# Performance work log

Measured on AMD Instinct MI355X. Metric: run time of the kernel, lower is better.

## Reference

```python
import jax, jax.numpy as jnp
import numpy as np

V, E, H = 30000, 512, 512
MARGIN = 0.05


def _lstm(x, wih, whh, b):
    # x: [N,T,E]; torch LSTM gate order i,f,g,o; returns outputs [N,T,H]
    N = x.shape[0]
    Hh = whh.shape[1]
    xproj = jnp.swapaxes(x, 0, 1) @ wih.T + b  # [T,N,4H], input proj hoisted out of scan

    def step(carry, xp):
        h, c = carry
        g = xp + h @ whh.T
        i, f, gg, o = jnp.split(g, 4, axis=-1)
        c = jax.nn.sigmoid(f) * c + jax.nn.sigmoid(i) * jnp.tanh(gg)
        h = jax.nn.sigmoid(o) * jnp.tanh(c)
        return (h, c), h

    h0 = jnp.zeros((N, Hh), x.dtype)
    _, hs = jax.lax.scan(step, (h0, h0), xproj)
    return jnp.swapaxes(hs, 0, 1)


def _attn_pool(feat, lengths, aw, ab, sw, sb):
    # batched masked-softmax attention pooling (replaces per-sample python loop)
    T = feat.shape[1]
    s = (jnp.tanh(feat @ aw.T + ab) @ sw.T + sb)[..., 0]  # [N,T]
    mask = jnp.arange(T)[None, :] < lengths[:, None]
    w = jax.nn.softmax(jnp.where(mask, s, -1e30), axis=1)
    return jnp.einsum('nt,nth->nh', w, feat)  # [N,H]


def _cos(a, b, eps=1e-8):
    na = jnp.maximum(jnp.linalg.norm(a, axis=-1), eps)
    nb = jnp.maximum(jnp.linalg.norm(b, axis=-1), eps)
    return jnp.sum(a * b, axis=-1) / (na * nb)


def setup_inputs() -> dict:
    key = jax.random.key(0)
    ks = jax.random.split(key, 24)
    B, BL, T, TD = 32, 8, 128, 256
    d = {}
    d['tran'] = jax.random.randint(ks[0], (B, BL, T), 1, V)
    d['tran_len'] = jax.random.randint(ks[1], (B,), 1, T + 1)
    d['tran_block_len'] = jax.random.randint(ks[2], (B, BL), 1, T + 1)
    d['doc_anchor'] = jax.random.randint(ks[3], (B, TD), 1, V)
    d['doc_anchor_len'] = jax.random.randint(ks[4], (B,), 1, TD + 1)
    d['doc_neg'] = jax.random.randint(ks[5], (B, TD), 1, V)
    d['doc_neg_len'] = jax.random.randint(ks[6], (B,), 1, TD + 1)
    sc = 0.05
    emb = jax.random.normal(ks[7], (V, E), jnp.float32) * sc
    d['emb'] = emb.at[0].set(0.0)  # padding_idx=0
    d['tran_wih'] = jax.random.normal(ks[8], (4 * H, E), jnp.float32) * sc
    d['tran_whh'] = jax.random.normal(ks[9], (4 * H, H), jnp.float32) * sc
    d['tran_b'] = jax.random.normal(ks[10], (4 * H,), jnp.float32) * sc
    d['doc_wih'] = jax.random.normal(ks[11], (4 * H, E), jnp.float32) * sc
    d['doc_whh'] = jax.random.normal(ks[12], (4 * H, H), jnp.float32) * sc
    d['doc_b'] = jax.random.normal(ks[13], (4 * H,), jnp.float32) * sc
    d['tran_attn_w'] = jax.random.normal(ks[14], (H, H), jnp.float32) * sc
    d['tran_attn_b'] = jax.random.normal(ks[15], (H,), jnp.float32) * sc
    d['tran_s_w'] = jax.random.normal(ks[16], (1, H), jnp.float32) * sc
    d['tran_s_b'] = jax.random.normal(ks[17], (1,), jnp.float32) * sc
    d['doc_attn_w'] = jax.random.normal(ks[18], (H, H), jnp.float32) * sc
    d['doc_attn_b'] = jax.random.normal(ks[19], (H,), jnp.float32) * sc
    d['doc_s_w'] = jax.random.normal(ks[20], (1, H), jnp.float32) * sc
    d['doc_s_b'] = jax.random.normal(ks[21], (1,), jnp.float32) * sc
    return d


def reference(tran, tran_len, tran_block_len, doc_anchor, doc_anchor_len,
              doc_neg, doc_neg_len, emb, tran_wih, tran_whh, tran_b,
              doc_wih, doc_whh, doc_b, tran_attn_w, tran_attn_b,
              tran_s_w, tran_s_b, doc_attn_w, doc_attn_b, doc_s_w, doc_s_b):
    B, BL, T = tran.shape
    # --- code side: encode B*BL sub-sequences, attn pool, tanh, max over block ---
    flat = tran.reshape(B * BL, T)
    feat = _lstm(emb[flat], tran_wih, tran_whh, tran_b)  # [B*BL,T,H]
    pooled = _attn_pool(feat, tran_block_len.reshape(-1),
                        tran_attn_w, tran_attn_b, tran_s_w, tran_s_b)
    pooled = jnp.tanh(pooled)  # use_tanh on attn output (tran path)
    code_repr = jnp.max(pooled.reshape(B, BL, H), axis=1)  # max_pool over block

    # --- doc side: attn pool, no trailing tanh (doc_encoding has no use_tanh branch) ---
    def doc_enc(tok, lens):
        f = _lstm(emb[tok], doc_wih, doc_whh, doc_b)
        return _attn_pool(f, lens, doc_attn_w, doc_attn_b, doc_s_w, doc_s_b)

    da = doc_enc(doc_anchor, doc_anchor_len)
    dn = doc_enc(doc_neg, doc_neg_len)

    anchor_sim = _cos(code_repr, da)
    neg_sim = _cos(code_repr, dn)
    loss = jnp.mean(jnp.clip(MARGIN - anchor_sim + neg_sim, 1e-6, None))
    return loss
```

## Files before the change

kernel.cpp:

```cpp
#include <hip/hip_runtime.h>
#include <hip/hip_bf16.h>

#define NSEQ 320
#define NTRAN 256
#define TT 128
#define TDOC 256
#define EH 512
#define XR_TRAN (NTRAN*TT)
#define XROWS (XR_TRAN + 64*TDOC)
#define HSLOTS 6
#define FW 264

typedef __attribute__((ext_vector_type(8))) short bf16x8v;
typedef __attribute__((ext_vector_type(4))) float f32x4v;

__device__ __align__(16) unsigned short g_xb [(size_t)XROWS*EH];
__device__ __align__(16) unsigned short g_wbx[2*2048*512];
__device__ __align__(16) unsigned short g_w2b[2*5*512*512];
__device__ float g_xp[(size_t)XROWS*2048];
__device__ float g_h [HSLOTS*NSEQ*EH];
__device__ float g_sc[64*260];
__device__ float g_pool[NSEQ*EH];
__device__ float g_loss;
__device__ unsigned g_gflag[48*FW];
__device__ unsigned g_sflag[16*FW];
__device__ unsigned g_aprog[48];

__device__ __forceinline__ float sigm(float x) { return 1.0f / (1.0f + expf(-x)); }

__device__ __forceinline__ float ldg_sys(const float* p) {
  return __hip_atomic_load(p, __ATOMIC_RELAXED, __HIP_MEMORY_SCOPE_SYSTEM);
}
__device__ __forceinline__ void stg_sys(float* p, float v) {
  __hip_atomic_store(p, v, __ATOMIC_RELAXED, __HIP_MEMORY_SCOPE_SYSTEM);
}
__device__ __forceinline__ unsigned ldu(const unsigned* p) {
  return __hip_atomic_load(p, __ATOMIC_RELAXED, __HIP_MEMORY_SCOPE_AGENT);
}
__device__ __forceinline__ unsigned short f2b(float f) {
  __hip_bfloat16 h = __float2bfloat16(f);
  return *reinterpret_cast<unsigned short*>(&h);
}

__global__ __launch_bounds__(256) void init_state() {
  int i = blockIdx.x*256 + threadIdx.x;
  if (i < NSEQ*EH) g_h[5*NSEQ*EH + i] = 0.0f;
  if (i < 64*260) g_sc[i] = 0.0f;
  if (i < 48*FW) g_gflag[i] = ((i % FW) == 0) ? 4u : 0u;
  if (i < 16*FW) g_sflag[i] = 0u;
  if (i < 48) g_aprog[i] = 0u;
  if (i == 0) g_loss = 0.0f;
}

__global__ __launch_bounds__(256) void build_wbx(
    const float* __restrict__ wih_t, const float* __restrict__ wih_d) {
  int idx = blockIdx.x*256 + threadIdx.x;
  if (idx >= 2*2048*512) return;
  int p = idx / (2048*512); int rem = idx % (2048*512);
  const float* wih = p ? wih_d : wih_t;
  g_wbx[idx] = f2b(wih[rem]);
}

__global__ __launch_bounds__(256) void build_wt2(
    const float* __restrict__ whh_t, const float* __restrict__ whh_d,
    const float* __restrict__ aw_t,  const float* __restrict__ aw_d) {
  int idx = blockIdx.x*256 + threadIdx.x;
  if (idx >= 2*5*512*512) return;
  int p  = idx / (5*512*512); int rem = idx % (5*512*512);
  int cg = rem / (512*512);   int r2  = rem % (512*512);
  int k  = r2 >> 9;           int c   = r2 & 511;
  float v;
  if (cg < 4) {
    int r = (c >> 7)*512 + cg*128 + (c & 127);
    const float* whh = p ? whh_d : whh_t;
    v = whh[r*512 + k];
  } else {
    const float* aw = p ? aw_d : aw_t;
    v = aw[c*512 + k];
  }
  g_w2b[((size_t)(p*5 + cg)*512 + k)*512 + c] = f2b(v);
}

__global__ __launch_bounds__(128) void pregather(
    const int* __restrict__ tran, const int* __restrict__ da_tok,
    const int* __restrict__ dn_tok, const float* __restrict__ emb) {
  int row = blockIdx.x;
  int tok;
  if (row < XR_TRAN) tok = tran[row];
  else {
    int q = row - XR_TRAN;
    tok = (q < 32*TDOC) ? da_tok[q] : dn_tok[q - 32*TDOC];
  }
  const float4* src = (const float4*)&emb[(size_t)tok*EH];
  float4 v = src[threadIdx.x];
  uint2 o;
  o.x = (unsigned)f2b(v.x) | ((unsigned)f2b(v.y) << 16);
  o.y = (unsigned)f2b(v.z) | ((unsigned)f2b(v.w) << 16);
  ((uint2*)&g_xb[(size_t)row*EH])[threadIdx.x] = o;
}

__global__ __launch_bounds__(512, 2) void xproj_mfma(
    const float* __restrict__ b_t, const float* __restrict__ b_d) {
  __shared__ short As[2][256*32];
  __shared__ short Bs[2][256*32];
  const int bid = blockIdx.x;
  const int mt = bid >> 3, ntb = bid & 7;
  const size_t mb = (size_t)mt * 256; const int nb = ntb * 256;
  const bool tp = (mb < XR_TRAN);
  const size_t wboff = (tp ? 0 : (size_t)2048*512);
  const float* __restrict__ bias = tp ? b_t : b_d;
  const int tid = threadIdx.x;
  const int l = tid & 63, w = tid >> 6;
  const int mw = w >> 2, nw = w & 3;

  f32x4v acc[8][4];
  #pragma unroll
  for (int m2 = 0; m2 < 8; ++m2)
    #pragma unroll
    for (int n2 = 0; n2 < 4; ++n2) acc[m2][n2] = (f32x4v){0.f, 0.f, 0.f, 0.f};

  uint4 rA[2], rB[2];
  auto stage_load = [&](int k0) {
    #pragma unroll
    for (int i = 0; i < 2; ++i) {
      int u = i*512 + tid;
      rA[i] = *(const uint4*)&g_xb[(mb + (u >> 2))*512 + k0 + (u & 3)*8];
      rB[i] = *(const uint4*)&g_wbx[wboff + (size_t)(nb + (u >> 2))*512 + k0 + (u & 3)*8];
    }
  };
  auto stage_write = [&](int buf) {
    #pragma unroll
    for (int i = 0; i < 2; ++i) {
      int u = i*512 + tid;
      *(uint4*)&As[buf][u*8] = rA[i];
      *(uint4*)&Bs[buf][u*8] = rB[i];
    }
  };

  stage_load(0); stage_write(0); __syncthreads();
  for (int ks = 0; ks < 16; ++ks) {
    const int buf = ks & 1;
    if (ks < 15) stage_load((ks + 1)*32);
    bf16x8v aF[8], bF[4];
    #pragma unroll
    for (int m2 = 0; m2 < 8; ++m2)
      aF[m2] = *(const bf16x8v*)&As[buf][(mw*128 + m2*16 + (l & 15))*32 + (l >> 4)*8];
    #pragma unroll
    for (int n2 = 0; n2 < 4; ++n2)
      bF[n2] = *(const bf16x8v*)&Bs[buf][(nw*64 + n2*16 + (l & 15))*32 + (l >> 4)*8];
    #pragma unroll
    for (int m2 = 0; m2 < 8; ++m2)
      #pragma unroll
      for (int n2 = 0; n2 < 4; ++n2)
        acc[m2][n2] = __builtin_amdgcn_mfma_f32_16x16x32_bf16(aF[m2], bF[n2], acc[m2][n2], 0, 0, 0);
    __syncthreads();
    if (ks < 15) stage_write(buf ^ 1);
    __syncthreads();
  }

  #pragma unroll
  for (int n2 = 0; n2 < 4; ++n2) {
    const int colg = nb + nw*64 + n2*16 + (l & 15);
    const int col2 = ((colg & 511) >> 7)*512 + (colg >> 9)*128 + (colg & 127);
    const float bv = bias[colg];
    #pragma unroll
    for (int m2 = 0; m2 < 8; ++m2) {
      #pragma unroll
      for (int r = 0; r < 4; ++r) {
        size_t row = mb + mw*128 + m2*16 + (l >> 4)*4 + r;
        g_xp[row*2048 + col2] = acc[m2][n2][r] + bv;
      }
    }
  }
}

template<int S, int CPL>
__device__ __forceinline__ void gemm2(const unsigned short* __restrict__ wsl,
                                      const float* __restrict__ ht,
                                      float* __restrict__ part,
                                      int kq, int lane) {
  constexpr int PW = CPL*64 + 4;
  float acc[CPL][S];
  #pragma unroll
  for (int c = 0; c < CPL; ++c)
    #pragma unroll
    for (int s = 0; s < S; ++s) acc[c][s] = 0.0f;
  const unsigned short* wp = wsl + (size_t)(kq*64)*512 + CPL*lane;
  const float* hb = ht + kq*64;
  #pragma unroll 2
  for (int k4 = 0; k4 < 16; ++k4) {
    float4 hv[S];
    #pragma unroll
    for (int s = 0; s < S; ++s) hv[s] = *(const float4*)&hb[s*516 + k4*4];
    #pragma unroll
    for (int i4 = 0; i4 < 4; ++i4) {
      float wf[CPL];
      if constexpr (CPL == 8) {
        uint4 wv = *(const uint4*)(wp + (size_t)(k4*4 + i4)*512);
        wf[0] = __uint_as_float(wv.x << 16); wf[1] = __uint_as_float(wv.x & 0xFFFF0000u);
        wf[2] = __uint_as_float(wv.y << 16); wf[3] = __uint_as_float(wv.y & 0xFFFF0000u);
        wf[4] = __uint_as_float(wv.z << 16); wf[5] = __uint_as_float(wv.z & 0xFFFF0000u);
        wf[6] = __uint_as_float(wv.w << 16); wf[7] = __uint_as_float(wv.w & 0xFFFF0000u);
      } else {
        uint2 wv = *(const uint2*)(wp + (size_t)(k4*4 + i4)*512);
        wf[0] = __uint_as_float(wv.x << 16); wf[1] = __uint_as_float(wv.x & 0xFFFF0000u);
        wf[2] = __uint_as_float(wv.y << 16); wf[3] = __uint_as_float(wv.y & 0xFFFF0000u);
      }
      #pragma unroll
      for (int s = 0; s < S; ++s) {
        float h = ((const float*)&hv[s])[i4];
        #pragma unroll
        for (int c = 0; c < CPL; ++c) acc[c][s] = fmaf(wf[c], h, acc[c][s]);
      }
    }
  }
  if (kq < 4) {
    #pragma unroll
    for (int s = 0; s < S; ++s)
      #pragma unroll
      for (int c = 0; c < CPL; ++c)
        part[(size_t)(kq*S + s)*PW + CPL*lane + c] = acc[c][s];
  }
  __syncthreads();
  if (kq >= 4) {
    const int q = kq - 4;
    #pragma unroll
    for (int s = 0; s < S; ++s)
      #pragma unroll
      for (int c = 0; c < CPL; ++c)
        part[(size_t)(q*S + s)*PW + CPL*lane + c] += acc[c][s];
  }
}

__global__ __launch_bounds__(512, 2) void persist(
    const int* __restrict__ tbl, const int* __restrict__ dal, const int* __restrict__ dnl,
    const float* __restrict__ ab_t, const float* __restrict__ ab_d,
    const float* __restrict__ sw_t, const float* __restrict__ sw_d,
    const float* __restrict__ sb_t, const float* __restrict__ sb_d) {
  __shared__ float sm[28920];
  float* part = sm;
  float* ht   = sm + 16512;
  float* cb   = sm + 20640;
  float* scr  = sm + 24736;
  float* ml   = sm + 24752;
  float* lenb = sm + 24768;
  float* alb  = sm + 24776;
  float* htB  = sm + 24792;

  const int b = blockIdx.x, tid = threadIdx.x;
  const int x = b & 7, m = b >> 3;
  bool tran; int cg, nt;
  if (x < 5) { tran = true; cg = x; nt = m; }
  else { int slot = (x - 5)*32 + m; tran = false; cg = slot >> 4; nt = slot & 15; }
  const int S     = tran ? 8 : 4;
  const int Ts    = tran ? TT : TDOC;
  const int sbase = tran ? nt*8 : NTRAN + nt*4;
  const bool isattn = (cg >= 4);
  const int gr = tran ? nt : 32 + nt;
  const unsigned AK = tran ? 1u : 2u;
  const int colbase = tran ? 0 : (cg - 4) * 256;
  const int wslice  = isattn ? 4 : cg;
  const unsigned short* __restrict__ wsl =
      g_w2b + (size_t)((tran ? 0 : 5) + wslice)*512*512 + (isattn ? colbase : 0);
  const float* __restrict__ ab  = tran ? ab_t : ab_d;
  const float* __restrict__ sw  = tran ? sw_t : sw_d;
  const float  sb = tran ? sb_t[0] : sb_d[0];

  for (int i = tid; i < 4096; i += 512) cb[i] = 0.0f;
  if (tid < S) {
    ml[tid*2] = -3.0e38f; ml[tid*2+1] = 0.0f;
    int s = sbase + tid;
    int len = tran ? tbl[s] : (s < NTRAN+32 ? dal[s-NTRAN] : dnl[s-NTRAN-32]);
    lenb[tid] = (float)len;
  }
  __syncthreads();

  const int lane = tid & 63, kq = tid >> 6;
  const int w = kq;
  const int PW = tran ? 516 : (isattn ? 260 : 516);
  const int CW = isattn ? (tran ? 512 : 256) : 0;
  const int DW = isattn ? (tran ? 512 : 256) : 0;

  if (!isattn) {
    for (int t = 0; t < Ts; ++t) {
      float xpA[4], xpB[4];
      {
        int i = tid; int jl = i & 127, s = i >> 7;
        size_t row = tran ? (size_t)(sbase + s)*TT + t
                          : (size_t)XR_TRAN + (size_t)(sbase + s - NTRAN)*TDOC + t;
        const float* xr = &g_xp[row*2048 + cg*512];
        #pragma unroll
        for (int g4 = 0; g4 < 4; ++g4) xpA[g4] = xr[g4*128 + jl];
      }
      if (tran) {
        int i = tid + 512; int jl = i & 127, s = i >> 7;
        size_t row = (size_t)(sbase + s)*TT + t;
        const float* xr = &g_xp[row*2048 + cg*512];
        #pragma unroll
        for (int g4 = 0; g4 < 4; ++g4) xpB[g4] = xr[g4*128 + jl];
      }
      if (t > 0)
        while (ldu(&g_gflag[gr*FW + t]) < 4u) __builtin_amdgcn_s_sleep(1);
      if (t >= 5) {
        unsigned tgt = AK * (unsigned)(t - 4);
        while (ldu(&g_aprog[gr]) < tgt) __builtin_amdgcn_s_sleep(1);
      }
      const int sp = (t + 5) % HSLOTS;
      for (int s = 0; s < S; ++s)
        ht[s*516 + kq*64 + lane] =
            ldg_sys(&g_h[((size_t)sp*NSEQ + sbase + s)*EH + kq*64 + lane]);
      if (tran) gemm2<8,8>(wsl, ht, part, kq, lane);
      else      gemm2<4,8>(wsl, ht, part, kq, lane);
      __syncthreads();
      const int so = t % HSLOTS;
      {
        int i = tid; int jl = i & 127, s = i >> 7;
        float u[4];
        #pragma unroll
        for (int g4 = 0; g4 < 4; ++g4) {
          float v = xpA[g4];
          #pragma unroll
          for (int q = 0; q < 4; ++q) v += part[(size_t)(q*S + s)*516 + g4*128 + jl];
          u[g4] = v;
        }
        float cv = cb[s*128 + jl];
        float cn = sigm(u[1])*cv + sigm(u[0])*tanhf(u[2]);
        float hn = sigm(u[3])*tanhf(cn);
        cb[s*128 + jl] = cn;
        stg_sys(&g_h[((size_t)so*NSEQ + sbase + s)*EH + cg*128 + jl], hn);
      }
      if (tran) {
        int i = tid + 512; int jl = i & 127, s = i >> 7;
        float u[4];
        #pragma unroll
        for (int g4 = 0; g4 < 4; ++g4) {
          float v = xpB[g4];
          #pragma unroll
          for (int q = 0; q < 4; ++q) v += part[(size_t)(q*S + s)*516 + g4*128 + jl];
          u[g4] = v;
        }
        float cv = cb[s*128 + jl];
        float cn = sigm(u[1])*cv + sigm(u[0])*tanhf(u[2]);
        float hn = sigm(u[3])*tanhf(cn);
        cb[s*128 + jl] = cn;
        stg_sys(&g_h[((size_t)so*NSEQ + sbase + s)*EH + cg*128 + jl], hn);
      }
      __syncthreads();
      if (tid == 0) atomicAdd(&g_gflag[gr*FW + t + 1], 1u);
    }
  } else {
    for (int t = 1; t <= Ts + 1; ++t) {
      float* hcur  = (t & 1) ? htB : ht;
      float* hprev = (t & 1) ? ht : htB;
      if (tid == 0) {
        if (t <= Ts)
          while (ldu(&g_gflag[gr*FW + t]) < 4u) __builtin_amdgcn_s_sleep(1);
        if (!tran && t >= 2)
          while (ldu(&g_sflag[nt*FW + (t - 1)]) < 2u) __builtin_amdgcn_s_sleep(1);
      }
      __syncthreads();
      const int sp = (t + 5) % HSLOTS;
      if (t <= Ts) {
        for (int s = 0; s < S; ++s)
          hcur[s*516 + kq*64 + lane] =
              ldg_sys(&g_h[((size_t)sp*NSEQ + sbase + s)*EH + kq*64 + lane]);
      }
      if (t >= 2 && tid < S) {
        int s = tid;
        if ((float)(t - 2) < lenb[s]) {
          float sv = tran ? scr[(t & 1)*8 + s]
                          : ldg_sys(&g_sc[(sbase + s - NTRAN)*260 + (t - 2)]);
          float mo = ml[s*2], lo = ml[s*2+1];
          float mn = fmaxf(mo, sv);
          float a = expf(mo - mn), e = expf(sv - mn);
          alb[s*2] = a; alb[s*2+1] = e;
          ml[s*2] = mn; ml[s*2+1] = lo*a + e;
        } else { alb[s*2] = 1.0f; alb[s*2+1] = 0.0f; }
      }
      __syncthreads();
      if (t <= Ts) {
        if (tran) gemm2<8,8>(wsl, hcur, part, kq, lane);
        else      gemm2<4,4>(wsl, hcur, part, kq, lane);
      }
      if (t >= 2) {
        for (int i = tid; i < S*DW; i += 512) {
          int s = tran ? (i >> 9) : (i >> 8);
          int dl = i & (DW - 1);
          float a = alb[s*2], e = alb[s*2+1];
          if (!(a == 1.0f && e == 0.0f)) {
            float hv = hprev[s*516 + colbase + dl];
            cb[s*DW + dl] = cb[s*DW + dl]*a + e*hv;
          }
        }
      }
      __syncthreads();
      if (tid == 0) atomicAdd(&g_aprog[gr], 1u);
      if (t <= Ts) {
        for (int i = tid; i < CW*S; i += 512) {
          int c = i & (CW - 1);
          int s = tran ? (i >> 9) : (i >> 8);
          float u = ab[colbase + c];
          #pragma unroll
          for (int q = 0; q < 4; ++q) u += part[(size_t)(q*S + s)*PW + c];
          float p = tanhf(u) * sw[colbase + c];
          part[(size_t)s*PW + c] = p;
        }
        __syncthreads();
        if (w < S) {
          int s = w;
          float p = 0.0f;
          for (int j = 0; j < CW/64; ++j) p += part[(size_t)s*PW + j*64 + lane];
          #pragma unroll
          for (int off = 32; off >= 1; off >>= 1) p += __shfl_xor(p, off, 64);
          if (lane == 0) {
            if (tran) scr[((t - 1) & 1)*8 + s] = p + sb;
            else atomicAdd(&g_sc[(sbase + s - NTRAN)*260 + (t - 1)],
                           p + (cg == 4 ? sb : 0.0f));
          }
        }
        if (!tran) {
          __syncthreads();
          if (tid == 0) atomicAdd(&g_sflag[nt*FW + t], 1u);
        }
      }
    }
    for (int i = tid; i < S*DW; i += 512) {
      int s = tran ? (i >> 9) : (i >> 8);
      int dl = i & (DW - 1);
      float v = cb[s*DW + dl] / ml[s*2+1];
      if (tran) v = tanhf(v);
      g_pool[(size_t)(sbase + s)*EH + colbase + dl] = v;
    }
  }
}

__global__ __launch_bounds__(256) void loss_partial() {
  __shared__ float red[5][4];
  int b = blockIdx.x, tid = threadIdx.x;
  float p[5] = {0.f, 0.f, 0.f, 0.f, 0.f};
  for (int j = tid; j < EH; j += 256) {
    float mx = -3.0e38f;
    #pragma unroll
    for (int bl = 0; bl < 8; bl++) mx = fmaxf(mx, g_pool[(b*8 + bl)*EH + j]);
    float da = g_pool[(NTRAN + b)*EH + j];
    float dn = g_pool[(NTRAN + 32 + b)*EH + j];
    p[0] += mx*mx; p[1] += da*da; p[2] += dn*dn; p[3] += mx*da; p[4] += mx*dn;
  }
  int lane = tid & 63, w = tid >> 6;
  #pragma unroll
  for (int i = 0; i < 5; i++) {
    float v = p[i];
    for (int off = 32; off >= 1; off >>= 1) v += __shfl_xor(v, off, 64);
    if (lane == 0) red[i][w] = v;
  }
  __syncthreads();
  if (tid == 0) {
    float cc = red[0][0]+red[0][1]+red[0][2]+red[0][3];
    float aa = red[1][0]+red[1][1]+red[1][2]+red[1][3];
    float nn = red[2][0]+red[2][1]+red[2][2]+red[2][3];
    float ca = red[3][0]+red[3][1]+red[3][2]+red[3][3];
    float cn = red[4][0]+red[4][1]+red[4][2]+red[4][3];
    float ncr = fmaxf(sqrtf(cc), 1e-8f);
    float nda = fmaxf(sqrtf(aa), 1e-8f);
    float ndn = fmaxf(sqrtf(nn), 1e-8f);
    float simA = ca / (ncr * nda);
    float simN = cn / (ncr * ndn);
    float term = fmaxf(0.05f - simA + simN, 1e-6f);
    atomicAdd(&g_loss, term * (1.0f / 32.0f));
  }
}

__global__ void write_out(float* __restrict__ out) {
  if (threadIdx.x == 0 && blockIdx.x == 0) out[0] = g_loss;
}

extern "C" void kernel_launch(void* const* d_in, const int* in_sizes, int n_in,
                              void* d_out, int out_size, void* d_ws, size_t ws_size,
                              hipStream_t stream) {
  (void)in_sizes; (void)n_in; (void)out_size; (void)d_ws; (void)ws_size;
  const int*   tran   = (const int*)d_in[0];
  const int*   tbl    = (const int*)d_in[2];
  const int*   da_tok = (const int*)d_in[3];
  const int*   dal    = (const int*)d_in[4];
  const int*   dn_tok = (const int*)d_in[5];
  const int*   dnl    = (const int*)d_in[6];
  const float* emb    = (const float*)d_in[7];
  const float* wih_t  = (const float*)d_in[8];
  const float* whh_t  = (const float*)d_in[9];
  const float* b_t    = (const float*)d_in[10];
  const float* wih_d  = (const float*)d_in[11];
  const float* whh_d  = (const float*)d_in[12];
  const float* b_d    = (const float*)d_in[13];
  const float* aw_t   = (const float*)d_in[14];
  const float* ab_t   = (const float*)d_in[15];
  const float* sw_t   = (const float*)d_in[16];
  const float* sb_t   = (const float*)d_in[17];
  const float* aw_d   = (const float*)d_in[18];
  const float* ab_d   = (const float*)d_in[19];
  const float* sw_d   = (const float*)d_in[20];
  const float* sb_d   = (const float*)d_in[21];

  init_state<<<(NSEQ*EH + 255)/256, 256, 0, stream>>>();
  build_wbx<<<(2*2048*512 + 255)/256, 256, 0, stream>>>(wih_t, wih_d);
  build_wt2<<<(2*5*512*512 + 255)/256, 256, 0, stream>>>(whh_t, whh_d, aw_t, aw_d);
  pregather<<<XROWS, 128, 0, stream>>>(tran, da_tok, dn_tok, emb);
  xproj_mfma<<<(XROWS/256)*8, 512, 0, stream>>>(b_t, b_d);

  persist<<<256, 512, 0, stream>>>(tbl, dal, dnl,
      ab_t, ab_d, sw_t, sw_d, sb_t, sb_d);

  loss_partial<<<32, 256, 0, stream>>>();
  write_out<<<1, 64, 0, stream>>>((float*)d_out);
}
```

Measured before the change: 2.990 ms.

## Replace scalar FMA recurrent GEMM with bf16 MFMA and bf16 hidden state

Result: slower. 4.689 ms (+56.8%).

```diff
diff --git a/kernel.cpp b/kernel.cpp
--- a/kernel.cpp
+++ b/kernel.cpp
@@ -41,6 +41,9 @@
   __hip_bfloat16 h = __float2bfloat16(f);
   return *reinterpret_cast<unsigned short*>(&h);
 }
+__device__ __forceinline__ float b2f(unsigned short u) {
+  return __uint_as_float((unsigned)u << 16);
+}
 
 __global__ __launch_bounds__(256) void init_state() {
   int i = blockIdx.x*256 + threadIdx.x;
@@ -68,7 +71,7 @@
   if (idx >= 2*5*512*512) return;
   int p  = idx / (5*512*512); int rem = idx % (5*512*512);
   int cg = rem / (512*512);   int r2  = rem % (512*512);
-  int k  = r2 >> 9;           int c   = r2 & 511;
+  int c  = r2 >> 9;           int k   = r2 & 511;
   float v;
   if (cg < 4) {
     int r = (c >> 7)*512 + cg*128 + (c & 127);
@@ -78,7 +81,7 @@
     const float* aw = p ? aw_d : aw_t;
     v = aw[c*512 + k];
   }
-  g_w2b[((size_t)(p*5 + cg)*512 + k)*512 + c] = f2b(v);
+  g_w2b[((size_t)(p*5 + cg)*512 + c)*512 + k] = f2b(v);
 }
 
 __global__ __launch_bounds__(128) void pregather(
@@ -174,61 +177,32 @@
   }
 }
 
-template<int S, int CPL>
-__device__ __forceinline__ void gemm2(const unsigned short* __restrict__ wsl,
-                                      const float* __restrict__ ht,
-                                      float* __restrict__ part,
-                                      int kq, int lane) {
-  constexpr int PW = CPL*64 + 4;
-  float acc[CPL][S];
+template<int NV, int NCT>
+__device__ __forceinline__ void gemm_mfma(const unsigned short* __restrict__ wcol,
+                                          const unsigned short* __restrict__ hB,
+                                          float* __restrict__ gates,
+                                          int w, int lane) {
+  const int sidx = lane & 15, klane = lane >> 4;
+  f32x4v acc[NCT];
   #pragma unroll
-  for (int c = 0; c < CPL; ++c)
-    #pragma unroll
-    for (int s = 0; s < S; ++s) acc[c][s] = 0.0f;
-  const unsigned short* wp = wsl + (size_t)(kq*64)*512 + CPL*lane;
-  const float* hb = ht + kq*64;
+  for (int i = 0; i < NCT; ++i) acc[i] = (f32x4v){0.f, 0.f, 0.f, 0.f};
+  const unsigned short* hrow = hB + sidx*512 + klane*8;
+  const unsigned short* wbaseL = wcol + (size_t)(w*NCT*16 + sidx)*512 + klane*8;
   #pragma unroll 2
-  for (int k4 = 0; k4 < 16; ++k4) {
-    float4 hv[S];
-    #pragma unroll
-    for (int s = 0; s < S; ++s) hv[s] = *(const float4*)&hb[s*516 + k4*4];
-    #pragma unroll
-    for (int i4 = 0; i4 < 4; ++i4) {
-      float wf[CPL];
-      if constexpr (CPL == 8) {
-        uint4 wv = *(const uint4*)(wp + (size_t)(k4*4 + i4)*512);
-        wf[0] = __uint_as_float(wv.x << 16); wf[1] = __uint_as_float(wv.x & 0xFFFF0000u);
-        wf[2] = __uint_as_float(wv.y << 16); wf[3] = __uint_as_float(wv.y & 0xFFFF0000u);
-        wf[4] = __uint_as_float(wv.z << 16); wf[5] = __uint_as_float(wv.z & 0xFFFF0000u);
-        wf[6] = __uint_as_float(wv.w << 16); wf[7] = __uint_as_float(wv.w & 0xFFFF0000u);
-      } else {
-        uint2 wv = *(const uint2*)(wp + (size_t)(k4*4 + i4)*512);
-        wf[0] = __uint_as_float(wv.x << 16); wf[1] = __uint_as_float(wv.x & 0xFFFF0000u);
-        wf[2] = __uint_as_float(wv.y << 16); wf[3] = __uint_as_float(wv.y & 0xFFFF0000u);
-      }
-      #pragma unroll
-      for (int s = 0; s < S; ++s) {
-        float h = ((const float*)&hv[s])[i4];
-        #pragma unroll
-        for (int c = 0; c < CPL; ++c) acc[c][s] = fmaf(wf[c], h, acc[c][s]);
-      }
-    }
-  }
-  if (kq < 4) {
-    #pragma unroll
-    for (int s = 0; s < S; ++s)
-      #pragma unroll
-      for (int c = 0; c < CPL; ++c)
-        part[(size_t)(kq*S + s)*PW + CPL*lane + c] = acc[c][s];
-  }
-  __syncthreads();
-  if (kq >= 4) {
-    const int q = kq - 4;
-    #pragma unroll
-    for (int s = 0; s < S; ++s)
-      #pragma unroll
-      for (int c = 0; c < CPL; ++c)
-        part[(size_t)(q*S + s)*PW + CPL*lane + c] += acc[c][s];
+  for (int ks = 0; ks < 16; ++ks) {
+    bf16x8v bF = *(const bf16x8v*)(hrow + ks*32);
+    #pragma unroll
+    for (int i = 0; i < NCT; ++i) {
+      bf16x8v aF = *(const bf16x8v*)(wbaseL + (size_t)i*16*512 + ks*32);
+      acc[i] = __builtin_amdgcn_mfma_f32_16x16x32_bf16(aF, bF, acc[i], 0, 0, 0);
+    }
+  }
+  if (sidx < NV) {
+    #pragma unroll
+    for (int i = 0; i < NCT; ++i) {
+      int cbase = (w*NCT + i)*16 + klane*4;
+      *(f32x4v*)&gates[sidx*516 + cbase] = acc[i];
+    }
   }
 }
 
@@ -237,15 +211,15 @@
     const float* __restrict__ ab_t, const float* __restrict__ ab_d,
     const float* __restrict__ sw_t, const float* __restrict__ sw_d,
     const float* __restrict__ sb_t, const float* __restrict__ sb_d) {
-  __shared__ float sm[28920];
-  float* part = sm;
-  float* ht   = sm + 16512;
-  float* cb   = sm + 20640;
-  float* scr  = sm + 24736;
-  float* ml   = sm + 24752;
-  float* lenb = sm + 24768;
-  float* alb  = sm + 24776;
-  float* htB  = sm + 24792;
+  __shared__ float sm[25600];
+  float* gates = sm;
+  float* cb    = sm + 4128;
+  unsigned short* hA  = (unsigned short*)(sm + 8224);
+  unsigned short* hB2 = (unsigned short*)(sm + 12320);
+  float* scr  = sm + 16416;
+  float* ml   = sm + 16432;
+  float* lenb = sm + 16448;
+  float* alb  = sm + 16456;
 
   const int b = blockIdx.x, tid = threadIdx.x;
   const int x = b & 7, m = b >> 3;
@@ -260,13 +234,14 @@
   const unsigned AK = tran ? 1u : 2u;
   const int colbase = tran ? 0 : (cg - 4) * 256;
   const int wslice  = isattn ? 4 : cg;
-  const unsigned short* __restrict__ wsl =
-      g_w2b + (size_t)((tran ? 0 : 5) + wslice)*512*512 + (isattn ? colbase : 0);
+  const unsigned short* __restrict__ wbase =
+      g_w2b + ((size_t)((tran ? 0 : 5) + wslice)*512 + (isattn ? colbase : 0))*512;
   const float* __restrict__ ab  = tran ? ab_t : ab_d;
   const float* __restrict__ sw  = tran ? sw_t : sw_d;
   const float  sb = tran ? sb_t[0] : sb_d[0];
 
   for (int i = tid; i < 4096; i += 512) cb[i] = 0.0f;
+  for (int i = tid; i < 1024; i += 512) { ((uint4*)hA)[i] = make_uint4(0,0,0,0); ((uint4*)hB2)[i] = make_uint4(0,0,0,0); }
   if (tid < S) {
     ml[tid*2] = -3.0e38f; ml[tid*2+1] = 0.0f;
     int s = sbase + tid;
@@ -275,11 +250,9 @@
   }
   __syncthreads();
 
-  const int lane = tid & 63, kq = tid >> 6;
-  const int w = kq;
-  const int PW = tran ? 516 : (isattn ? 260 : 516);
+  const int lane = tid & 63, w = tid >> 6;
   const int CW = isattn ? (tran ? 512 : 256) : 0;
-  const int DW = isattn ? (tran ? 512 : 256) : 0;
+  const int DW = CW;
 
   if (!isattn) {
     for (int t = 0; t < Ts; ++t) {
@@ -306,23 +279,24 @@
         while (ldu(&g_aprog[gr]) < tgt) __builtin_amdgcn_s_sleep(1);
       }
       const int sp = (t + 5) % HSLOTS;
-      for (int s = 0; s < S; ++s)
-        ht[s*516 + kq*64 + lane] =
-            ldg_sys(&g_h[((size_t)sp*NSEQ + sbase + s)*EH + kq*64 + lane]);
-      if (tran) gemm2<8,8>(wsl, ht, part, kq, lane);
-      else      gemm2<4,8>(wsl, ht, part, kq, lane);
+      for (int i = tid; i < S*64; i += 512) {
+        int s = i >> 6, k8 = (i & 63)*8;
+        const float* hsrc = &g_h[((size_t)sp*NSEQ + sbase + s)*EH + k8];
+        unsigned short tmp[8];
+        #pragma unroll
+        for (int j = 0; j < 8; ++j) tmp[j] = f2b(ldg_sys(hsrc + j));
+        *(uint4*)&hA[s*512 + k8] = *(const uint4*)tmp;
+      }
+      __syncthreads();
+      if (tran) gemm_mfma<8,4>(wbase, hA, gates, w, lane);
+      else      gemm_mfma<4,4>(wbase, hA, gates, w, lane);
       __syncthreads();
       const int so = t % HSLOTS;
       {
         int i = tid; int jl = i & 127, s = i >> 7;
         float u[4];
         #pragma unroll
-        for (int g4 = 0; g4 < 4; ++g4) {
-          float v = xpA[g4];
-          #pragma unroll
-          for (int q = 0; q < 4; ++q) v += part[(size_t)(q*S + s)*516 + g4*128 + jl];
-          u[g4] = v;
-        }
+        for (int g4 = 0; g4 < 4; ++g4) u[g4] = xpA[g4] + gates[s*516 + g4*128 + jl];
         float cv = cb[s*128 + jl];
         float cn = sigm(u[1])*cv + sigm(u[0])*tanhf(u[2]);
         float hn = sigm(u[3])*tanhf(cn);
@@ -333,12 +307,7 @@
         int i = tid + 512; int jl = i & 127, s = i >> 7;
         float u[4];
         #pragma unroll
-        for (int g4 = 0; g4 < 4; ++g4) {
-          float v = xpB[g4];
-          #pragma unroll
-          for (int q = 0; q < 4; ++q) v += part[(size_t)(q*S + s)*516 + g4*128 + jl];
-          u[g4] = v;
-        }
+        for (int g4 = 0; g4 < 4; ++g4) u[g4] = xpB[g4] + gates[s*516 + g4*128 + jl];
         float cv = cb[s*128 + jl];
         float cn = sigm(u[1])*cv + sigm(u[0])*tanhf(u[2]);
         float hn = sigm(u[3])*tanhf(cn);
@@ -350,8 +319,8 @@
     }
   } else {
     for (int t = 1; t <= Ts + 1; ++t) {
-      float* hcur  = (t & 1) ? htB : ht;
-      float* hprev = (t & 1) ? ht : htB;
+      unsigned short* hcur  = (t & 1) ? hB2 : hA;
+      unsigned short* hprev = (t & 1) ? hA : hB2;
       if (tid == 0) {
         if (t <= Ts)
           while (ldu(&g_gflag[gr*FW + t]) < 4u) __builtin_amdgcn_s_sleep(1);
@@ -361,9 +330,14 @@
       __syncthreads();
       const int sp = (t + 5) % HSLOTS;
       if (t <= Ts) {
-        for (int s = 0; s < S; ++s)
-          hcur[s*516 + kq*64 + lane] =
-              ldg_sys(&g_h[((size_t)sp*NSEQ + sbase + s)*EH + kq*64 + lane]);
+        for (int i = tid; i < S*64; i += 512) {
+          int s = i >> 6, k8 = (i & 63)*8;
+          const float* hsrc = &g_h[((size_t)sp*NSEQ + sbase + s)*EH + k8];
+          unsigned short tmp[8];
+          #pragma unroll
+          for (int j = 0; j < 8; ++j) tmp[j] = f2b(ldg_sys(hsrc + j));
+          *(uint4*)&hcur[s*512 + k8] = *(const uint4*)tmp;
+        }
       }
       if (t >= 2 && tid < S) {
         int s = tid;
@@ -379,8 +353,8 @@
       }
       __syncthreads();
       if (t <= Ts) {
-        if (tran) gemm2<8,8>(wsl, hcur, part, kq, lane);
-        else      gemm2<4,4>(wsl, hcur, part, kq, lane);
+        if (tran) gemm_mfma<8,4>(wbase, hcur, gates, w, lane);
+        else      gemm_mfma<4,2>(wbase, hcur, gates, w, lane);
       }
       if (t >= 2) {
         for (int i = tid; i < S*DW; i += 512) {
@@ -388,7 +362,7 @@
           int dl = i & (DW - 1);
           float a = alb[s*2], e = alb[s*2+1];
           if (!(a == 1.0f && e == 0.0f)) {
-            float hv = hprev[s*516 + colbase + dl];
+            float hv = b2f(hprev[s*512 + colbase + dl]);
             cb[s*DW + dl] = cb[s*DW + dl]*a + e*hv;
           }
         }
@@ -399,17 +373,15 @@
         for (int i = tid; i < CW*S; i += 512) {
           int c = i & (CW - 1);
           int s = tran ? (i >> 9) : (i >> 8);
-          float u = ab[colbase + c];
-          #pragma unroll
-          for (int q = 0; q < 4; ++q) u += part[(size_t)(q*S + s)*PW + c];
+          float u = ab[colbase + c] + gates[s*516 + c];
           float p = tanhf(u) * sw[colbase + c];
-          part[(size_t)s*PW + c] = p;
+          gates[s*516 + c] = p;
         }
         __syncthreads();
         if (w < S) {
           int s = w;
           float p = 0.0f;
-          for (int j = 0; j < CW/64; ++j) p += part[(size_t)s*PW + j*64 + lane];
+          for (int j = 0; j < CW/64; ++j) p += gates[s*516 + j*64 + lane];
           #pragma unroll
           for (int off = 32; off >= 1; off >>= 1) p += __shfl_xor(p, off, 64);
           if (lane == 0) {
```

## Regroup doc LSTM blocks to eight sequences per group, idling surplus blocks

Applied to the files above, without the earlier changes.

New measurement: 4.849 ms. 1.62x slower.

```diff
diff --git a/kernel.cpp b/kernel.cpp
--- a/kernel.cpp
+++ b/kernel.cpp
@@ -251,14 +251,20 @@
   const int x = b & 7, m = b >> 3;
   bool tran; int cg, nt;
   if (x < 5) { tran = true; cg = x; nt = m; }
-  else { int slot = (x - 5)*32 + m; tran = false; cg = slot >> 4; nt = slot & 15; }
-  const int S     = tran ? 8 : 4;
+  else {
+    int slot = (x - 5) + 3*m;
+    if (slot >= 48) return;
+    tran = false;
+    nt = slot / 6; int role = slot % 6;
+    cg = role;
+  }
+  const int S     = 8;
   const int Ts    = tran ? TT : TDOC;
-  const int sbase = tran ? nt*8 : NTRAN + nt*4;
+  const int sbase = tran ? nt*8 : NTRAN + nt*8;
   const bool isattn = (cg >= 4);
   const int gr = tran ? nt : 32 + nt;
   const unsigned AK = tran ? 1u : 2u;
-  const int colbase = tran ? 0 : (cg - 4) * 256;
+  const int colbase = tran ? 0 : (isattn ? (cg - 4)*256 : 0);
   const int wslice  = isattn ? 4 : cg;
   const unsigned short* __restrict__ wsl =
       g_w2b + (size_t)((tran ? 0 : 5) + wslice)*512*512 + (isattn ? colbase : 0);
@@ -277,9 +283,9 @@
 
   const int lane = tid & 63, kq = tid >> 6;
   const int w = kq;
-  const int PW = tran ? 516 : (isattn ? 260 : 516);
+  const int PW = isattn ? (tran ? 516 : 260) : 516;
   const int CW = isattn ? (tran ? 512 : 256) : 0;
-  const int DW = isattn ? (tran ? 512 : 256) : 0;
+  const int DW = CW;
 
   if (!isattn) {
     for (int t = 0; t < Ts; ++t) {
@@ -292,9 +298,10 @@
         #pragma unroll
         for (int g4 = 0; g4 < 4; ++g4) xpA[g4] = xr[g4*128 + jl];
       }
-      if (tran) {
+      {
         int i = tid + 512; int jl = i & 127, s = i >> 7;
-        size_t row = (size_t)(sbase + s)*TT + t;
+        size_t row = tran ? (size_t)(sbase + s)*TT + t
+                          : (size_t)XR_TRAN + (size_t)(sbase + s - NTRAN)*TDOC + t;
         const float* xr = &g_xp[row*2048 + cg*512];
         #pragma unroll
         for (int g4 = 0; g4 < 4; ++g4) xpB[g4] = xr[g4*128 + jl];
@@ -309,32 +316,16 @@
       for (int s = 0; s < S; ++s)
         ht[s*516 + kq*64 + lane] =
             ldg_sys(&g_h[((size_t)sp*NSEQ + sbase + s)*EH + kq*64 + lane]);
-      if (tran) gemm2<8,8>(wsl, ht, part, kq, lane);
-      else      gemm2<4,8>(wsl, ht, part, kq, lane);
+      gemm2<8,8>(wsl, ht, part, kq, lane);
       __syncthreads();
       const int so = t % HSLOTS;
-      {
-        int i = tid; int jl = i & 127, s = i >> 7;
+      #pragma unroll
+      for (int ch2 = 0; ch2 < 2; ++ch2) {
+        int i = tid + ch2*512; int jl = i & 127, s = i >> 7;
         float u[4];
         #pragma unroll
         for (int g4 = 0; g4 < 4; ++g4) {
-          float v = xpA[g4];
-          #pragma unroll
-          for (int q = 0; q < 4; ++q) v += part[(size_t)(q*S + s)*516 + g4*128 + jl];
-          u[g4] = v;
-        }
-        float cv = cb[s*128 + jl];
-        float cn = sigm(u[1])*cv + sigm(u[0])*tanhf(u[2]);
-        float hn = sigm(u[3])*tanhf(cn);
-        cb[s*128 + jl] = cn;
-        stg_sys(&g_h[((size_t)so*NSEQ + sbase + s)*EH + cg*128 + jl], hn);
-      }
-      if (tran) {
-        int i = tid + 512; int jl = i & 127, s = i >> 7;
-        float u[4];
-        #pragma unroll
-        for (int g4 = 0; g4 < 4; ++g4) {
-          float v = xpB[g4];
+          float v = ch2 ? xpB[g4] : xpA[g4];
           #pragma unroll
           for (int q = 0; q < 4; ++q) v += part[(size_t)(q*S + s)*516 + g4*128 + jl];
           u[g4] = v;
@@ -380,7 +371,7 @@
       __syncthreads();
       if (t <= Ts) {
         if (tran) gemm2<8,8>(wsl, hcur, part, kq, lane);
-        else      gemm2<4,4>(wsl, hcur, part, kq, lane);
+        else      gemm2<8,4>(wsl, hcur, part, kq, lane);
       }
       if (t >= 2) {
         for (int i = tid; i < S*DW; i += 512) {
```
